# Optimization experiments

Hardware: AMD Instinct MI355X
Metric: run time of the kernel (lower is better)

The kernel has to match this reference:

```python
import jax, jax.numpy as jnp
import numpy as np

B, T, D, H, C = 128, 256, 64, 512, 10
MISSING = 128.0
LAMDA = 1.0
REG_COEF = 0.0001


def setup_inputs() -> dict:
    key = jax.random.key(0)
    ks = jax.random.split(key, 10)
    x = jax.random.normal(ks[0], (B, T, D), dtype=jnp.float32)
    miss = jax.random.uniform(ks[1], (B, T, D)) < 0.2
    x = jnp.where(miss, jnp.float32(MISSING), x)
    prediction_target = jax.random.normal(ks[2], (B, T - 1, D), dtype=jnp.float32)
    mask = (jax.random.uniform(ks[3], (B, T - 1, D)) < 0.8).astype(jnp.float32)
    labels = jax.random.randint(ks[4], (B,), 0, C)
    label_target = jax.nn.one_hot(labels, C, dtype=jnp.float32)
    # projection params (truncated normal stddev 0.1, bias 0.1 as in source)
    W = jax.random.truncated_normal(ks[5], -2.0, 2.0, (H, D), dtype=jnp.float32) * 0.1
    bias = jnp.full((D,), 0.1, dtype=jnp.float32)
    # LSTMCell params: kernel [D,4H], recurrent kernel [H,4H], bias [4H] (gate order i,f,g,o)
    kernel = jax.random.normal(ks[6], (D, 4 * H), dtype=jnp.float32) * 0.05
    rkernel = jax.random.normal(ks[7], (H, 4 * H), dtype=jnp.float32) * 0.05
    lstm_bias = jnp.zeros((4 * H,), dtype=jnp.float32)
    dense_W = jax.random.normal(ks[8], (H, C), dtype=jnp.float32) * 0.05
    dense_b = jnp.zeros((C,), dtype=jnp.float32)
    return {"input": x, "prediction_target": prediction_target, "mask": mask,
            "label_target": label_target, "W": W, "bias": bias, "kernel": kernel,
            "rkernel": rkernel, "lstm_bias": lstm_bias, "dense_W": dense_W,
            "dense_b": dense_b}


def reference(input, prediction_target, mask, label_target, W, bias,
              kernel, rkernel, lstm_bias, dense_W, dense_b):
    def lstm_cell(h, c, x):
        z = x @ kernel + h @ rkernel + lstm_bias  # [B,4H]
        i, f, g, o = jnp.split(z, 4, axis=-1)
        c_new = jax.nn.sigmoid(f) * c + jax.nn.sigmoid(i) * jnp.tanh(g)
        h_new = jax.nn.sigmoid(o) * jnp.tanh(c_new)
        return h_new, c_new

    h0 = jnp.zeros((B, H), dtype=input.dtype)
    c0 = jnp.zeros((B, H), dtype=input.dtype)
    # step 0: raw input, no imputation
    h1, c1 = lstm_cell(h0, c0, input[:, 0, :])

    def step(carry, x_t):
        h, c = carry
        pred = h @ W + bias  # imputation from previous output
        x_in = jnp.where(x_t == MISSING, pred, x_t)
        h, c = lstm_cell(h, c, x_in)
        return (h, c), h

    xs = jnp.swapaxes(input[:, 1:, :], 0, 1)  # [T-1,B,D]
    (_, _), hs = jax.lax.scan(step, (h1, c1), xs)  # hs: [T-1,B,H]
    outputs = jnp.concatenate([h1[None], hs], axis=0)  # [T,B,H]

    # prediction branch: outputs[:-1] -> project to input space
    pred_hidden = jnp.swapaxes(outputs[:-1], 0, 1).reshape(-1, H)  # [B*(T-1),H]
    prediction = pred_hidden @ W + bias  # [B*(T-1),D]
    targets = prediction_target.reshape(-1, D)
    masks = mask.reshape(-1, D)
    loss_prediction = jnp.mean(jnp.square((targets - prediction) * masks)) / B

    # classification branch on last hidden state
    logits = outputs[-1] @ dense_W + dense_b  # [B,C]
    loss_classification = -jnp.sum(label_target * jax.nn.log_softmax(logits), axis=-1)  # [B]

    # L2 regularization over all variables (tf.nn.l2_loss = sum(x^2)/2)
    params = (W, bias, kernel, rkernel, lstm_bias, dense_W, dense_b)
    reg = sum(0.5 * jnp.sum(jnp.square(p)) for p in params)

    loss = loss_classification + LAMDA * loss_prediction + REG_COEF * reg  # [B]
    return loss
```

## Files before the change

kernel.cpp:

```cpp
#include <hip/hip_runtime.h>
#include <math.h>

constexpr int Bb = 128, Tt = 256, Dd = 64, Hh = 512, Cc = 10;
constexpr float MISSINGV = 128.0f;

#define NBLK 256
#define NTHR 256

typedef float v4f __attribute__((ext_vector_type(4)));
typedef float f4 __attribute__((ext_vector_type(4)));
typedef _Float16 half8 __attribute__((ext_vector_type(8)));
typedef _Float16 half4 __attribute__((ext_vector_type(4)));

constexpr size_t WS_PLOSS = 128;
constexpr size_t WS_REG   = 192;
constexpr size_t WS_FLG   = 256;
constexpr size_t WS_H     = 8192;
constexpr size_t WS_WT16  = WS_H + 262144;
constexpr size_t WS_BM16  = WS_WT16 + 65536;

constexpr int XSTR = 72;
constexpr int PSTR = 68;
constexpr int HSTR = 520;
constexpr size_t SM_XIN  = 0;
constexpr size_t SM_PRED = 2304;
constexpr size_t SM_ZS   = 6656;
constexpr size_t SM_RED  = 11008;
constexpr size_t SM_H    = 11072;
constexpr size_t SM_TOTAL= SM_H + (size_t)16 * HSTR * 2;

#define CLD4O(dst, base, OFF) \
    asm volatile("global_load_dwordx4 %0, %1, off offset:" OFF " sc0 sc1" : "=v"(dst) : "v"(base))
#define CWAIT4(a0,a1,a2,a3) \
    asm volatile("s_waitcnt vmcnt(0)" : "+v"(a0),"+v"(a1),"+v"(a2),"+v"(a3) :: "memory")

__device__ __forceinline__ unsigned coh_ld_u(const unsigned* p) {
    return __hip_atomic_load(p, __ATOMIC_RELAXED, __HIP_MEMORY_SCOPE_AGENT);
}
__device__ __forceinline__ void coh_st_u(unsigned* p, unsigned v) {
    __hip_atomic_store(p, v, __ATOMIC_RELAXED, __HIP_MEMORY_SCOPE_AGENT);
}
__device__ __forceinline__ float fsig(float v)  { return __builtin_amdgcn_rcpf(1.f + __expf(-v)); }
__device__ __forceinline__ float ftanh(float v) { float e = __expf(2.f*v); return 1.f - 2.f*__builtin_amdgcn_rcpf(e+1.f); }

__global__ void prep_weights(const float* __restrict__ rk, const float* __restrict__ kern,
                             const float* __restrict__ W,
                             _Float16* __restrict__ bm, _Float16* __restrict__ wt) {
    int o = blockIdx.x * 256 + threadIdx.x;
    if (o < 32 * 64 * 576) {
        int ht = o / 36864, rem = o % 36864, n = rem / 576, k = rem % 576;
        int u = n >> 2, g = n & 3, col = g * 512 + ht * 16 + u;
        float v = (k < 64) ? kern[k * 2048 + col] : rk[(k - 64) * 2048 + col];
        bm[o] = (_Float16)v;
    }
    if (o < 64 * 512) {
        int d = o >> 9, k = o & 511;
        wt[o] = (_Float16)W[k * 64 + d];
    }
}

__launch_bounds__(NTHR, 1)
__global__ void ajrnn_persistent(
    const float* __restrict__ x, const float* __restrict__ tgt, const float* __restrict__ msk,
    const float* __restrict__ W, const float* __restrict__ bias,
    const float* __restrict__ kern, const float* __restrict__ rkern, const float* __restrict__ lbias,
    const float* __restrict__ dW, const float* __restrict__ db,
    unsigned char* __restrict__ ws)
{
    __shared__ __align__(16) unsigned char smem[SM_TOTAL];
    _Float16* xinS = (_Float16*)(smem + SM_XIN);
    float* predS = (float*)(smem + SM_PRED);
    float* zS    = (float*)(smem + SM_ZS);
    float* redsc = (float*)(smem + SM_RED);
    _Float16* hS = (_Float16*)(smem + SM_H);

    float* ploss_acc = (float*)(ws + WS_PLOSS);
    float* reg_acc   = (float*)(ws + WS_REG);
    _Float16* h16h   = (_Float16*)(ws + WS_H);
    unsigned* h16u   = (unsigned*)(ws + WS_H);
    const _Float16* WT16g = (const _Float16*)(ws + WS_WT16);
    const _Float16* BM16g = (const _Float16*)(ws + WS_BM16);

    const int tid = threadIdx.x;
    const int bid = blockIdx.x;
    const int rt = bid >> 5, ht = bid & 31;
    const int r0 = rt * 16, j0 = ht * 16;
    const int wave = tid >> 6, lane = tid & 63;
    const int lm = lane & 15;
    const int kq = (lane >> 4) * 8;
    const int cn = wave * 16 + lm;
    const int cr = tid >> 4, cu = tid & 15;

    unsigned* flg = (unsigned*)(ws + WS_FLG + (size_t)rt * 512);
    auto flag_wait = [&](unsigned t) {
        for (;;) {
            unsigned f = coh_ld_u(&flg[lane & 31]);
            if (__all((int)(f >= t))) break;
            __builtin_amdgcn_s_sleep(1);
        }
    };

    const float bvp = bias[cn];
    const int ju = j0 + cu;
    const float lb0 = lbias[ju], lb1 = lbias[Hh + ju], lb2 = lbias[2*Hh + ju], lb3 = lbias[3*Hh + ju];

    {
        float rs = 0.f;
        const float* arrs[7] = {W, bias, kern, rkern, lbias, dW, db};
        const int lens[7] = {Hh*Dd, Dd, Dd*4*Hh, Hh*4*Hh, 4*Hh, Hh*Cc, Cc};
        for (int a = 0; a < 7; ++a) {
            const float* p = arrs[a]; const int n = lens[a];
            for (int i = bid * NTHR + tid; i < n; i += NBLK * NTHR) { float v = p[i]; rs += v * v; }
        }
        #pragma unroll
        for (int off = 32; off > 0; off >>= 1) rs += __shfl_down(rs, off);
        if (lane == 0) redsc[wave] = rs;
        __syncthreads();
        if (tid == 0) atomicAdd(reg_acc, redsc[0] + redsc[1] + redsc[2] + redsc[3]);
        __syncthreads();
    }

    half8 b_z[18], b_p[16];
    {
        const _Float16* bmg = BM16g + ((size_t)ht * 64 + cn) * 576 + kq;
        const _Float16* wtg = WT16g + (size_t)cn * 512 + kq;
        #pragma unroll
        for (int kk = 0; kk < 18; ++kk) b_z[kk] = *(const half8*)(bmg + kk * 32);
        #pragma unroll
        for (int kk = 0; kk < 16; ++kk) b_p[kk] = *(const half8*)(wtg + kk * 32);
    }

    float c_reg = 0.f;
    float lacc = 0.f;

    auto gates_pub = [&](f4 zacc, unsigned* hwu, unsigned tpub) {
        const int prow = (lane >> 4) * 4;
        #pragma unroll
        for (int r = 0; r < 4; ++r) zS[(prow + r) * PSTR + cn] = zacc[r];
        __syncthreads();
        float4 zv = *(const float4*)&zS[cr * PSTR + cu * 4];
        float si = fsig(zv.x + lb0), sf = fsig(zv.y + lb1), so = fsig(zv.w + lb3);
        c_reg = sf * c_reg + si * ftanh(zv.z + lb2);
        float hv = so * ftanh(c_reg);
        float hv1 = __shfl_down(hv, 1);
        if (!(cu & 1)) {
            auto p = __builtin_amdgcn_cvt_pkrtz(hv, hv1);
            coh_st_u(&hwu[(size_t)(r0 + cr) * 256 + ((j0 + cu) >> 1)],
                     __builtin_bit_cast(unsigned, p));
        }
        asm volatile("s_waitcnt vmcnt(0)" ::: "memory");
        __syncthreads();
        if (tid == 0) coh_st_u(&flg[ht], tpub);
    };

    {
        const int rr = tid >> 4, dq = (tid & 15) * 4;
        float4 xv = *(const float4*)&x[((size_t)(r0 + rr) * Tt + 0) * Dd + dq];
        half4 xh; xh[0]=(_Float16)xv.x; xh[1]=(_Float16)xv.y; xh[2]=(_Float16)xv.z; xh[3]=(_Float16)xv.w;
        *(half4*)&xinS[rr * XSTR + dq] = xh;
        __syncthreads();
        half8 ax0 = *(const half8*)&xinS[lm * XSTR + kq];
        half8 ax1 = *(const half8*)&xinS[lm * XSTR + 32 + kq];
        f4 zacc = {0.f, 0.f, 0.f, 0.f};
        zacc = __builtin_amdgcn_mfma_f32_16x16x32_f16(ax0, b_z[0], zacc, 0, 0, 0);
        zacc = __builtin_amdgcn_mfma_f32_16x16x32_f16(ax1, b_z[1], zacc, 0, 0, 0);
        gates_pub(zacc, h16u, 1u);
    }

    for (int t = 1; t < Tt; ++t) {
        const _Float16* hr = h16h + ((t - 1) & 1) * (size_t)65536;
        unsigned*       hwu = h16u + (t & 1) * (size_t)32768;

        const int rr = tid >> 4, dq = (tid & 15) * 4;
        float4 xv = *(const float4*)&x[((size_t)(r0 + rr) * Tt + t) * Dd + dq];
        float tg = 0.f, mkv = 0.f;
        if (wave == 0 && lane < 32) {
            size_t ix = ((size_t)(r0 + (lane & 15)) * (Tt - 1) + (t - 1)) * Dd + 2*ht + (lane >> 4);
            tg = tgt[ix]; mkv = msk[ix];
        }

        flag_wait((unsigned)t);

        {
            const char* hb = (const char*)hr + ((size_t)r0 << 10) + (size_t)tid * 64;
            v4f s0, s1, s2, s3;
            CLD4O(s0, hb, "0"); CLD4O(s1, hb, "16"); CLD4O(s2, hb, "32"); CLD4O(s3, hb, "48");
            CWAIT4(s0, s1, s2, s3);
            _Float16* dst = hS + (size_t)(tid >> 4) * HSTR + (size_t)(tid & 15) * 32;
            *(half8*)(dst)      = __builtin_bit_cast(half8, s0);
            *(half8*)(dst + 8)  = __builtin_bit_cast(half8, s1);
            *(half8*)(dst + 16) = __builtin_bit_cast(half8, s2);
            *(half8*)(dst + 24) = __builtin_bit_cast(half8, s3);
        }
        __syncthreads();

        half8 ah[16];
        {
            const _Float16* hp = hS + (size_t)lm * HSTR + kq;
            #pragma unroll
            for (int j = 0; j < 16; ++j) ah[j] = *(const half8*)(hp + j * 32);
        }

        {
            f4 p0 = {0.f, 0.f, 0.f, 0.f}, p1 = {0.f, 0.f, 0.f, 0.f};
            #pragma unroll
            for (int kk = 0; kk < 16; kk += 2) {
                p0 = __builtin_amdgcn_mfma_f32_16x16x32_f16(ah[kk],     b_p[kk],     p0, 0, 0, 0);
                p1 = __builtin_amdgcn_mfma_f32_16x16x32_f16(ah[kk + 1], b_p[kk + 1], p1, 0, 0, 0);
            }
            f4 pacc = p0 + p1;
            const int prow = (lane >> 4) * 4;
            #pragma unroll
            for (int r = 0; r < 4; ++r) predS[(prow + r) * PSTR + cn] = pacc[r] + bvp;
        }
        __syncthreads();

        {
            float4 pv = *(const float4*)&predS[rr * PSTR + dq];
            half4 xh;
            xh[0] = (_Float16)((xv.x == MISSINGV) ? pv.x : xv.x);
            xh[1] = (_Float16)((xv.y == MISSINGV) ? pv.y : xv.y);
            xh[2] = (_Float16)((xv.z == MISSINGV) ? pv.z : xv.z);
            xh[3] = (_Float16)((xv.w == MISSINGV) ? pv.w : xv.w);
            *(half4*)&xinS[rr * XSTR + dq] = xh;
            if (wave == 0 && lane < 32) {
                float p = predS[(lane & 15) * PSTR + 2*ht + (lane >> 4)];
                float e = (tg - p) * mkv;
                lacc += e * e;
            }
        }
        __syncthreads();

        {
            half8 ax0 = *(const half8*)&xinS[lm * XSTR + kq];
            half8 ax1 = *(const half8*)&xinS[lm * XSTR + 32 + kq];
            f4 z0 = {0.f, 0.f, 0.f, 0.f}, z1 = {0.f, 0.f, 0.f, 0.f};
            #pragma unroll
            for (int kk = 0; kk < 16; kk += 2) {
                z0 = __builtin_amdgcn_mfma_f32_16x16x32_f16(ah[kk],     b_z[kk + 2], z0, 0, 0, 0);
                z1 = __builtin_amdgcn_mfma_f32_16x16x32_f16(ah[kk + 1], b_z[kk + 3], z1, 0, 0, 0);
            }
            z0 = __builtin_amdgcn_mfma_f32_16x16x32_f16(ax0, b_z[0], z0, 0, 0, 0);
            z1 = __builtin_amdgcn_mfma_f32_16x16x32_f16(ax1, b_z[1], z1, 0, 0, 0);
            gates_pub(z0 + z1, hwu, (unsigned)(t + 1));
        }
    }

    if (wave == 0) {
        #pragma unroll
        for (int off = 16; off > 0; off >>= 1) lacc += __shfl_down(lacc, off);
        if (lane == 0) atomicAdd(ploss_acc, lacc);
    }
}

__global__ void finalize(const float* __restrict__ lbl, const float* __restrict__ dW,
                         const float* __restrict__ db, float* __restrict__ out,
                         unsigned char* __restrict__ ws)
{
    __shared__ float dwl[Hh * Cc];
    const int tid = threadIdx.x;
    for (int i = tid; i < Hh * Cc; i += 128) dwl[i] = dW[i];
    __syncthreads();
    const float* ploss_acc = (const float*)(ws + WS_PLOSS);
    const float* reg_acc   = (const float*)(ws + WS_REG);
    const _Float16* h_last = (const _Float16*)(ws + WS_H) + 65536;

    if (tid < Bb) {
        float a[Cc];
        #pragma unroll
        for (int c = 0; c < Cc; ++c) a[c] = db[c];
        const _Float16* hrow = h_last + (size_t)tid * Hh;
        for (int k = 0; k < Hh; k += 8) {
            half8 hh = *(const half8*)(hrow + k);
            #pragma unroll
            for (int j = 0; j < 8; ++j) {
                float hv = (float)hh[j];
                #pragma unroll
                for (int c = 0; c < Cc; ++c) a[c] += hv * dwl[(k + j) * Cc + c];
            }
        }
        float m = a[0];
        #pragma unroll
        for (int c = 1; c < Cc; ++c) m = fmaxf(m, a[c]);
        float s = 0.f;
        #pragma unroll
        for (int c = 0; c < Cc; ++c) s += expf(a[c] - m);
        float lse = m + logf(s);
        float lc = 0.f;
        #pragma unroll
        for (int c = 0; c < Cc; ++c) lc += lbl[tid * Cc + c] * (lse - a[c]);
        float pl = ploss_acc[0];
        float rg = reg_acc[0];
        out[tid] = lc + pl * (1.0f / (2088960.0f * 128.0f)) + 1e-4f * 0.5f * rg;
    }
}

extern "C" void kernel_launch(void* const* d_in, const int* in_sizes, int n_in,
                              void* d_out, int out_size, void* d_ws, size_t ws_size,
                              hipStream_t stream) {
    const float* x     = (const float*)d_in[0];
    const float* tgt   = (const float*)d_in[1];
    const float* msk   = (const float*)d_in[2];
    const float* lbl   = (const float*)d_in[3];
    const float* W     = (const float*)d_in[4];
    const float* bias  = (const float*)d_in[5];
    const float* kern  = (const float*)d_in[6];
    const float* rkern = (const float*)d_in[7];
    const float* lbias = (const float*)d_in[8];
    const float* dW    = (const float*)d_in[9];
    const float* db    = (const float*)d_in[10];
    unsigned char* ws  = (unsigned char*)d_ws;

    (void)hipMemsetAsync(d_ws, 0, 8192, stream);
    prep_weights<<<4608, 256, 0, stream>>>(rkern, kern, W,
                                           (_Float16*)(ws + WS_BM16), (_Float16*)(ws + WS_WT16));
    ajrnn_persistent<<<NBLK, NTHR, 0, stream>>>(x, tgt, msk, W, bias, kern, rkern, lbias,
                                                dW, db, ws);
    finalize<<<1, 128, 0, stream>>>(lbl, dW, db, (float*)d_out, ws);
}
```

Measured before the change: 911.4 us.

## Remap blocks by XCC so h exchange stays in local L2; hoist recurrent MFMAs

At startup each block reads its hardware XCC id and takes a per-XCC rank through atomics, then all blocks wait at a one-time barrier. If every XCC holds exactly 32 blocks, the row tile is set to the XCC id, so every block sharing h for a row tile runs on the same XCC. Those blocks then exchange h with L2-scoped loads and stores (sc0 only) instead of going to memory-wide coherence (sc0 sc1). The h@rkernel MFMAs also move ahead of the prediction/imputation stage so they overlap with it. The one-time barrier adds startup cost, and the code relies on the hardware placing blocks evenly across XCCs, with a fallback to the old mapping if it does not.

Result: faster. 729.6 us (-20.0%).

```diff
diff --git a/kernel.cpp b/kernel.cpp
--- a/kernel.cpp
+++ b/kernel.cpp
@@ -15,6 +15,8 @@
 constexpr size_t WS_PLOSS = 128;
 constexpr size_t WS_REG   = 192;
 constexpr size_t WS_FLG   = 256;
+constexpr size_t WS_XC    = 4352;
+constexpr size_t WS_ARR   = 4416;
 constexpr size_t WS_H     = 8192;
 constexpr size_t WS_WT16  = WS_H + 262144;
 constexpr size_t WS_BM16  = WS_WT16 + 65536;
@@ -29,17 +31,13 @@
 constexpr size_t SM_H    = 11072;
 constexpr size_t SM_TOTAL= SM_H + (size_t)16 * HSTR * 2;
 
-#define CLD4O(dst, base, OFF) \
+#define CLD4O_MALL(dst, base, OFF) \
     asm volatile("global_load_dwordx4 %0, %1, off offset:" OFF " sc0 sc1" : "=v"(dst) : "v"(base))
+#define CLD4O_L2(dst, base, OFF) \
+    asm volatile("global_load_dwordx4 %0, %1, off offset:" OFF " sc0" : "=v"(dst) : "v"(base))
 #define CWAIT4(a0,a1,a2,a3) \
     asm volatile("s_waitcnt vmcnt(0)" : "+v"(a0),"+v"(a1),"+v"(a2),"+v"(a3) :: "memory")
 
-__device__ __forceinline__ unsigned coh_ld_u(const unsigned* p) {
-    return __hip_atomic_load(p, __ATOMIC_RELAXED, __HIP_MEMORY_SCOPE_AGENT);
-}
-__device__ __forceinline__ void coh_st_u(unsigned* p, unsigned v) {
-    __hip_atomic_store(p, v, __ATOMIC_RELAXED, __HIP_MEMORY_SCOPE_AGENT);
-}
 __device__ __forceinline__ float fsig(float v)  { return __builtin_amdgcn_rcpf(1.f + __expf(-v)); }
 __device__ __forceinline__ float ftanh(float v) { float e = __expf(2.f*v); return 1.f - 2.f*__builtin_amdgcn_rcpf(e+1.f); }
 
@@ -68,6 +66,7 @@
     unsigned char* __restrict__ ws)
 {
     __shared__ __align__(16) unsigned char smem[SM_TOTAL];
+    __shared__ int gS[3];
     _Float16* xinS = (_Float16*)(smem + SM_XIN);
     float* predS = (float*)(smem + SM_PRED);
     float* zS    = (float*)(smem + SM_ZS);
@@ -83,18 +82,42 @@
 
     const int tid = threadIdx.x;
     const int bid = blockIdx.x;
-    const int rt = bid >> 5, ht = bid & 31;
-    const int r0 = rt * 16, j0 = ht * 16;
     const int wave = tid >> 6, lane = tid & 63;
     const int lm = lane & 15;
     const int kq = (lane >> 4) * 8;
     const int cn = wave * 16 + lm;
     const int cr = tid >> 4, cu = tid & 15;
 
+    {
+        unsigned* xcnt = (unsigned*)(ws + WS_XC);
+        unsigned* arr  = (unsigned*)(ws + WS_ARR);
+        if (tid == 0) {
+            unsigned xcc;
+            asm volatile("s_getreg_b32 %0, hwreg(HW_REG_XCC_ID)" : "=s"(xcc));
+            xcc &= 7u;
+            unsigned rk = __hip_atomic_fetch_add(&xcnt[xcc], 1u, __ATOMIC_RELAXED, __HIP_MEMORY_SCOPE_AGENT);
+            __hip_atomic_fetch_add(arr, 1u, __ATOMIC_RELEASE, __HIP_MEMORY_SCOPE_AGENT);
+            while (__hip_atomic_load(arr, __ATOMIC_ACQUIRE, __HIP_MEMORY_SCOPE_AGENT) < (unsigned)NBLK)
+                __builtin_amdgcn_s_sleep(4);
+            int ok = 1;
+            for (int i = 0; i < 8; ++i)
+                ok &= (__hip_atomic_load(&xcnt[i], __ATOMIC_RELAXED, __HIP_MEMORY_SCOPE_AGENT) == 32u);
+            gS[0] = (int)xcc; gS[1] = (int)rk; gS[2] = ok;
+        }
+        __syncthreads();
+    }
+    const int l2m = gS[2];
+    const int rt = l2m ? gS[0] : (bid >> 5);
+    const int ht = l2m ? gS[1] : (bid & 31);
+    const int r0 = rt * 16, j0 = ht * 16;
+
     unsigned* flg = (unsigned*)(ws + WS_FLG + (size_t)rt * 512);
     auto flag_wait = [&](unsigned t) {
+        const unsigned* fp = &flg[lane & 31];
         for (;;) {
-            unsigned f = coh_ld_u(&flg[lane & 31]);
+            unsigned f;
+            asm volatile("global_load_dword %0, %1, off sc0 sc1\n\ts_waitcnt vmcnt(0)"
+                         : "=v"(f) : "v"(fp) : "memory");
             if (__all((int)(f >= t))) break;
             __builtin_amdgcn_s_sleep(1);
         }
@@ -145,12 +168,17 @@
         float hv1 = __shfl_down(hv, 1);
         if (!(cu & 1)) {
             auto p = __builtin_amdgcn_cvt_pkrtz(hv, hv1);
-            coh_st_u(&hwu[(size_t)(r0 + cr) * 256 + ((j0 + cu) >> 1)],
-                     __builtin_bit_cast(unsigned, p));
+            unsigned* hp = &hwu[(size_t)(r0 + cr) * 256 + ((j0 + cu) >> 1)];
+            unsigned pv = __builtin_bit_cast(unsigned, p);
+            if (l2m) asm volatile("global_store_dword %0, %1, off sc0"     :: "v"(hp), "v"(pv) : "memory");
+            else     asm volatile("global_store_dword %0, %1, off sc0 sc1" :: "v"(hp), "v"(pv) : "memory");
         }
         asm volatile("s_waitcnt vmcnt(0)" ::: "memory");
         __syncthreads();
-        if (tid == 0) coh_st_u(&flg[ht], tpub);
+        if (tid == 0) {
+            unsigned* fp = &flg[ht];
+            asm volatile("global_store_dword %0, %1, off sc0 sc1" :: "v"(fp), "v"(tpub) : "memory");
+        }
     };
 
     {
@@ -184,7 +212,10 @@
         {
             const char* hb = (const char*)hr + ((size_t)r0 << 10) + (size_t)tid * 64;
             v4f s0, s1, s2, s3;
-            CLD4O(s0, hb, "0"); CLD4O(s1, hb, "16"); CLD4O(s2, hb, "32"); CLD4O(s3, hb, "48");
+            if (l2m) { CLD4O_L2(s0, hb, "0");   CLD4O_L2(s1, hb, "16");
+                       CLD4O_L2(s2, hb, "32");  CLD4O_L2(s3, hb, "48"); }
+            else     { CLD4O_MALL(s0, hb, "0");  CLD4O_MALL(s1, hb, "16");
+                       CLD4O_MALL(s2, hb, "32"); CLD4O_MALL(s3, hb, "48"); }
             CWAIT4(s0, s1, s2, s3);
             _Float16* dst = hS + (size_t)(tid >> 4) * HSTR + (size_t)(tid & 15) * 32;
             *(half8*)(dst)      = __builtin_bit_cast(half8, s0);
@@ -201,12 +232,15 @@
             for (int j = 0; j < 16; ++j) ah[j] = *(const half8*)(hp + j * 32);
         }
 
+        f4 z0 = {0.f, 0.f, 0.f, 0.f}, z1 = {0.f, 0.f, 0.f, 0.f};
         {
             f4 p0 = {0.f, 0.f, 0.f, 0.f}, p1 = {0.f, 0.f, 0.f, 0.f};
             #pragma unroll
             for (int kk = 0; kk < 16; kk += 2) {
                 p0 = __builtin_amdgcn_mfma_f32_16x16x32_f16(ah[kk],     b_p[kk],     p0, 0, 0, 0);
                 p1 = __builtin_amdgcn_mfma_f32_16x16x32_f16(ah[kk + 1], b_p[kk + 1], p1, 0, 0, 0);
+                z0 = __builtin_amdgcn_mfma_f32_16x16x32_f16(ah[kk],     b_z[kk + 2], z0, 0, 0, 0);
+                z1 = __builtin_amdgcn_mfma_f32_16x16x32_f16(ah[kk + 1], b_z[kk + 3], z1, 0, 0, 0);
             }
             f4 pacc = p0 + p1;
             const int prow = (lane >> 4) * 4;
@@ -234,12 +268,6 @@
         {
             half8 ax0 = *(const half8*)&xinS[lm * XSTR + kq];
             half8 ax1 = *(const half8*)&xinS[lm * XSTR + 32 + kq];
-            f4 z0 = {0.f, 0.f, 0.f, 0.f}, z1 = {0.f, 0.f, 0.f, 0.f};
-            #pragma unroll
-            for (int kk = 0; kk < 16; kk += 2) {
-                z0 = __builtin_amdgcn_mfma_f32_16x16x32_f16(ah[kk],     b_z[kk + 2], z0, 0, 0, 0);
-                z1 = __builtin_amdgcn_mfma_f32_16x16x32_f16(ah[kk + 1], b_z[kk + 3], z1, 0, 0, 0);
-            }
             z0 = __builtin_amdgcn_mfma_f32_16x16x32_f16(ax0, b_z[0], z0, 0, 0, 0);
             z1 = __builtin_amdgcn_mfma_f32_16x16x32_f16(ax1, b_z[1], z1, 0, 0, 0);
             gates_pub(z0 + z1, hwu, (unsigned)(t + 1));
```
